# Kernel optimization log

Hardware: AMD Instinct MI355X
Metric: run time of the kernel (lower is better)

## Reference

```python
import jax, jax.numpy as jnp
import numpy as np

B, C, H, W = 4, 64, 64, 64  # x shape; mask is (B,1,8H,8W)


def _conv(x, w, pad=0):
    return jax.lax.conv_general_dilated(
        x, w, (1, 1), [(pad, pad), (pad, pad)],
        dimension_numbers=('NCHW', 'OIHW', 'NCHW'))


def _inorm(x, eps=1e-5):  # InstanceNorm2d, affine=False, biased var (torch default)
    mu = x.mean(axis=(2, 3), keepdims=True)
    var = x.var(axis=(2, 3), keepdims=True)
    return (x - mu) * jax.lax.rsqrt(var + eps)


def _forward(x, mask, kconv_w1, kconv_w2, fs_w1, fs_w2, fs_b2, fs_fuse_w):
    b, c, h, w = x.shape
    n = h * w
    # MaxPool2d(8,8) then binarize
    m = jax.lax.reduce_window(mask, -jnp.inf, jax.lax.max,
                              (1, 1, 8, 8), (1, 1, 8, 8), 'VALID')
    m = (m > 0).astype(x.dtype)
    back = 1.0 - m
    # ResidualBlock K_conv (shared for K and Q paths in original code)
    y = jax.nn.relu(_inorm(_conv(x, kconv_w1, pad=1)))
    y = _inorm(_conv(y, kconv_w2, pad=1))
    kx = jax.nn.relu(y + x)
    # L2-normalized K/Q over channel dim
    K = (kx * back).reshape(b, c, n)
    K = K / (jnp.linalg.norm(K, axis=1, keepdims=True) + 1e-8)
    Q = (kx * m).reshape(b, c, n)
    Q = Q / (jnp.linalg.norm(Q, axis=1, keepdims=True) + 1e-8)
    V = (x * back).reshape(b, c, n)
    # cosine-similarity score map, temperature 20
    score = jnp.einsum('bcq,bck->bqk', Q, K) * 20.0  # (b, n_q, n_k)
    qm = m.reshape(b, 1, n)      # query mask (foreground)
    km = back.reshape(b, 1, n)   # key mask (background)
    NEG = -1000000.0
    validx = score + (1.0 - km) * NEG + (1.0 - qm.transpose(0, 2, 1)) * NEG
    att = jax.nn.softmax(validx, axis=-1) * (qm.transpose(0, 2, 1) * km)
    # att_fore[b,c,q] = sum_k V[b,c,k] * att[b,q,k]
    att_fore = jnp.einsum('bck,bqk->bcq', V, att).reshape(b, c, h, w)
    # Fusion_score
    feat1 = _conv(jnp.concatenate([x * m, att_fore * m], axis=1), fs_w1)
    s = jax.nn.sigmoid(_conv(feat1, fs_w2) + fs_b2[None, :, None, None])
    fused = _conv(jnp.concatenate([x * m, att_fore * m * (1.0 - s)], axis=1), fs_fuse_w)
    fs_out = fused * m + x * (1.0 - m)
    out = fs_out * m + x * (1.0 - m)
    # visualization attention mask
    visatt = att.sum(axis=1).reshape(b, 1, h, w)
    attmask = jnp.repeat(jnp.repeat(visatt, 8, axis=2), 8, axis=3)  # nearest upsample x8
    attmask = attmask / attmask.max()
    return out, attmask


def setup_inputs() -> dict:
    key = jax.random.key(0)
    ks = jax.random.split(key, 8)

    def wgt(k, shape, fan_in):
        return jax.random.normal(k, shape, jnp.float32) / np.sqrt(fan_in)

    x = jax.random.normal(ks[0], (B, C, H, W), jnp.float32)
    # sparse foreground mask so maxpool(8x8)>0 yields a mixed fg/bg mask
    mask = (jax.random.uniform(ks[1], (B, 1, H * 8, W * 8)) < 0.01).astype(jnp.float32)
    return dict(
        x=x, mask=mask,
        kconv_w1=wgt(ks[2], (C, C, 3, 3), C * 9),
        kconv_w2=wgt(ks[3], (C, C, 3, 3), C * 9),
        fs_w1=wgt(ks[4], (C, 2 * C, 1, 1), 2 * C),
        fs_w2=wgt(ks[5], (C, C, 1, 1), C),
        fs_b2=jnp.zeros((C,), jnp.float32),
        fs_fuse_w=wgt(ks[6], (C, 2 * C, 1, 1), 2 * C),
    )


def reference(x, mask, kconv_w1, kconv_w2, fs_w1, fs_w2, fs_b2, fs_fuse_w):
    return _forward(x, mask, kconv_w1, kconv_w2, fs_w1, fs_w2, fs_b2, fs_fuse_w)
```

## Files before the change

### kernel.cpp

```cpp
#include <hip/hip_runtime.h>
#include <hip/hip_bf16.h>

typedef __hip_bfloat16 bf16;
typedef __attribute__((ext_vector_type(8))) short short8;
typedef __attribute__((ext_vector_type(4))) float f32x4;
typedef __attribute__((ext_vector_type(16))) float f32x16;

#define BB 4
#define CC 64
#define NN 4096
#define MH 512
#define MW 512
#define LS 72
#define NPARTS 16
#define NDEN 16

#define WB_AFC  ((size_t)0)
#define WB_VIS  ((size_t)4259840)
#define WB_QIX  ((size_t)4325376)
#define WB_KIX  ((size_t)4390912)
#define WB_MFL  ((size_t)4456448)
#define WB_CNT  ((size_t)4472832)
#define WB_WT1  ((size_t)4476992)
#define WB_WT2  ((size_t)4550720)
#define WB_WFB  ((size_t)4624448)
#define WB_KC   ((size_t)5242880)
#define WB_XT   ((size_t)8388608)
#define WB_KXT  ((size_t)10485760)
#define WB_VC   ((size_t)12582912)
#define WB_QC   ((size_t)14680064)
#define WB_E    ((size_t)16777216)
#define EB_ELEM ((size_t)16777216)
#define WB_AFCP ((size_t)150994944)
#define WB_DENP ((size_t)218103808)
#define WB_VISP ((size_t)220200960)
#define WB_GST  ((size_t)220725248)

__device__ __forceinline__ float us2f(unsigned short u) { return __uint_as_float(((unsigned)u) << 16); }
__device__ __forceinline__ unsigned short f2bu(float f) {
  bf16 h = __float2bfloat16(f);
  return *(unsigned short*)&h;
}

__global__ __launch_bounds__(256) void k_pre(const float* __restrict__ x,
                                             const float* __restrict__ mask,
                                             const float* __restrict__ w1,
                                             const float* __restrict__ w2,
                                             const float* __restrict__ fw1,
                                             const float* __restrict__ fw2,
                                             const float* __restrict__ fwf,
                                             float* __restrict__ outp,
                                             unsigned short* __restrict__ xt,
                                             unsigned char* __restrict__ mfl,
                                             float* __restrict__ vis,
                                             unsigned int* __restrict__ vmaxb,
                                             unsigned short* __restrict__ wT1,
                                             unsigned short* __restrict__ wT2,
                                             unsigned short* __restrict__ wfb) {
  __shared__ float lx[64][65];
  int t = threadIdx.x;
  if (blockIdx.x < 256) {
    int b = blockIdx.x >> 6, p0 = (blockIdx.x & 63) * 64;
    const float* xb = x + (size_t)b * CC * NN + p0;
    float* ob = outp + (size_t)b * CC * NN + p0;
    for (int idx = t; idx < 4096; idx += 256) {
      int c = idx >> 6, j = idx & 63;
      float v = xb[c * NN + j];
      lx[j][c] = v;
      ob[c * NN + j] = v;
    }
    __syncthreads();
    unsigned short* xo = xt + ((size_t)b * NN + p0) * 64;
    for (int idx = t; idx < 2048; idx += 256) {
      int j = idx >> 5, c2 = (idx & 31) * 2;
      ushort2 w2v;
      w2v.x = f2bu(lx[j][c2]);
      w2v.y = f2bu(lx[j][c2 + 1]);
      *(ushort2*)&xo[j * 64 + c2] = w2v;
    }
  } else {
    int g = (blockIdx.x - 256) * 256 + t;
    int o = g >> 2, sub = g & 3;
    int b = o >> 12, p = o & 4095;
    int py = p >> 6, px = p & 63;
    const float* mb = mask + (size_t)b * MH * MW + (py * 8 + sub * 2) * MW + px * 8;
    float mx = 0.f;
    #pragma unroll
    for (int dy = 0; dy < 2; ++dy) {
      const float4* r4 = (const float4*)(mb + dy * MW);
      float4 a = r4[0], c = r4[1];
      mx = fmaxf(mx, fmaxf(fmaxf(a.x, a.y), fmaxf(a.z, a.w)));
      mx = fmaxf(mx, fmaxf(fmaxf(c.x, c.y), fmaxf(c.z, c.w)));
    }
    mx = fmaxf(mx, __shfl_xor(mx, 1));
    mx = fmaxf(mx, __shfl_xor(mx, 2));
    if (sub == 0) {
      mfl[o] = (mx > 0.f) ? 1 : 0;
      vis[o] = 0.f;
    }
    if (g == 0) vmaxb[0] = 0u;
    if (g < 36864) {
      int tap = g >> 12;
      int rem = g & 4095;
      int co = rem >> 6, ci = rem & 63;
      int src = (co * 64 + ci) * 9 + tap;
      wT1[g] = f2bu(w1[src]);
      wT2[g] = f2bu(w2[src]);
    } else if (g < 57344) {
      int j2 = g - 36864;
      if (j2 < 8192)       wfb[j2] = f2bu(fw1[j2]);
      else if (j2 < 12288) wfb[j2] = f2bu(fw2[j2 - 8192]);
      else                 wfb[j2] = f2bu(fwf[j2 - 12288]);
    }
  }
}

__global__ __launch_bounds__(256) void k_compact(const unsigned char* __restrict__ mfl,
                                                 int* __restrict__ qidx, int* __restrict__ kidx,
                                                 int* __restrict__ nq, int* __restrict__ nk) {
  int b = blockIdx.x;
  __shared__ unsigned char lm[4096];
  int t = threadIdx.x;
  *(uint4*)&lm[t * 16] = *(const uint4*)&mfl[b * NN + t * 16];
  __syncthreads();
  if (t >= 64) return;
  int lane = t;
  int qb = 0, kb = 0;
  #pragma unroll
  for (int it = 0; it < 64; ++it) {
    int p = it * 64 + lane;
    bool f = lm[p] != 0;
    unsigned long long bal = __ballot(f);
    int before = __popcll(bal & ((1ULL << lane) - 1ULL));
    if (f)  qidx[b * NN + qb + before] = p;
    if (!f) kidx[b * NN + kb + (lane - before)] = p;
    int cnt = __popcll(bal);
    qb += cnt; kb += 64 - cnt;
  }
  if (lane == 0) { nq[b] = qb; nk[b] = kb; }
}

template <bool NORM_IN>
__global__ __launch_bounds__(256) void k_convm(const unsigned short* __restrict__ src,
                                               const unsigned short* __restrict__ wT,
                                               const float* __restrict__ insum,
                                               const float* __restrict__ insq,
                                               unsigned short* __restrict__ dst,
                                               float* __restrict__ gsump,
                                               float* __restrict__ gsqp) {
  int b = blockIdx.y;
  int r = blockIdx.x;
  __shared__ unsigned short bx[198 * LS];
  __shared__ float nmean[64], ninv[64];
  int t = threadIdx.x;
  if (NORM_IN) {
    if (t < 64) {
      float s = 0.f, s2v = 0.f;
      #pragma unroll 8
      for (int r2 = 0; r2 < 64; ++r2) {
        s   += insum[((size_t)r2 * BB + b) * 64 + t];
        s2v += insq [((size_t)r2 * BB + b) * 64 + t];
      }
      float m = s * (1.f / NN);
      float v = fmaxf(s2v * (1.f / NN) - m * m, 0.f);
      nmean[t] = m; ninv[t] = rsqrtf(v + 1e-5f);
    }
    __syncthreads();
  }
  const unsigned short* sb = src + (size_t)b * NN * 64;
  for (int idx = t; idx < 198 * 8; idx += 256) {
    int row = idx >> 3, c8 = (idx & 7) * 8;
    int dy = row / 66;
    int cx = row - dy * 66 - 1;
    int rr = r + dy - 1;
    uint4 v = make_uint4(0u, 0u, 0u, 0u);
    if ((unsigned)rr < 64u && (unsigned)cx < 64u) {
      v = *(const uint4*)(sb + ((size_t)(rr * 64 + cx)) * 64 + c8);
      if (NORM_IN) {
        unsigned short* e = (unsigned short*)&v;
        #pragma unroll
        for (int j = 0; j < 8; ++j)
          e[j] = f2bu(fmaxf((us2f(e[j]) - nmean[c8 + j]) * ninv[c8 + j], 0.f));
      }
    }
    *(uint4*)&bx[row * LS + c8] = v;
  }
  __syncthreads();
  int lane = t & 63;
  int quad = lane >> 4, col = lane & 15;
  int qw = (t >> 6) * 16;
  f32x4 acc[4] = {{0.f,0.f,0.f,0.f},{0.f,0.f,0.f,0.f},{0.f,0.f,0.f,0.f},{0.f,0.f,0.f,0.f}};
  #pragma unroll
  for (int tap = 0; tap < 9; ++tap) {
    int dy = tap / 3, dx = tap - dy * 3 - 1;
    const unsigned short* wrow = wT + ((size_t)tap * 64 + qw + col) * 64;
    short8 a0 = *(const short8*)(wrow + quad * 8);
    short8 a1 = *(const short8*)(wrow + 32 + quad * 8);
    int rbase = dy * 66 + dx + 1;
    #pragma unroll
    for (int nt = 0; nt < 4; ++nt) {
      int row = rbase + nt * 16 + col;
      short8 b0 = *(const short8*)&bx[row * LS + quad * 8];
      short8 b1 = *(const short8*)&bx[row * LS + 32 + quad * 8];
      acc[nt] = __builtin_amdgcn_mfma_f32_16x16x32_bf16(a0, b0, acc[nt], 0, 0, 0);
      acc[nt] = __builtin_amdgcn_mfma_f32_16x16x32_bf16(a1, b1, acc[nt], 0, 0, 0);
    }
  }
  #pragma unroll
  for (int rr = 0; rr < 4; ++rr) {
    float s1 = acc[0][rr] + acc[1][rr] + acc[2][rr] + acc[3][rr];
    float s2 = acc[0][rr]*acc[0][rr] + acc[1][rr]*acc[1][rr]
             + acc[2][rr]*acc[2][rr] + acc[3][rr]*acc[3][rr];
    s1 += __shfl_xor(s1, 1); s2 += __shfl_xor(s2, 1);
    s1 += __shfl_xor(s1, 2); s2 += __shfl_xor(s2, 2);
    s1 += __shfl_xor(s1, 4); s2 += __shfl_xor(s2, 4);
    s1 += __shfl_xor(s1, 8); s2 += __shfl_xor(s2, 8);
    if (col == 0) {
      int co = qw + quad * 4 + rr;
      gsump[((size_t)r * BB + b) * 64 + co] = s1;
      gsqp [((size_t)r * BB + b) * 64 + co] = s2;
    }
  }
  __syncthreads();
  #pragma unroll
  for (int nt = 0; nt < 4; ++nt)
    #pragma unroll
    for (int rr = 0; rr < 4; ++rr)
      bx[(nt * 16 + col) * LS + qw + quad * 4 + rr] = f2bu(acc[nt][rr]);
  __syncthreads();
  unsigned short* db = dst + ((size_t)b * NN + r * 64) * 64;
  for (int idx = t; idx < 512; idx += 256) {
    int px = idx >> 3, c8 = (idx & 7) * 8;
    *(uint4*)(db + (size_t)px * 64 + c8) = *(const uint4*)&bx[px * LS + c8];
  }
}

__global__ __launch_bounds__(256) void k_knorm(unsigned short* __restrict__ kxt,
                                               const unsigned short* __restrict__ xt,
                                               const float* __restrict__ gsump,
                                               const float* __restrict__ gsqp) {
  int b = blockIdx.x >> 6;
  int p0 = (blockIdx.x & 63) * 64;
  __shared__ float m2[64], i2[64];
  int t = threadIdx.x;
  if (t < 64) {
    float s = 0.f, s2v = 0.f;
    #pragma unroll 8
    for (int r2 = 0; r2 < 64; ++r2) {
      s   += gsump[((size_t)r2 * BB + b) * 64 + t];
      s2v += gsqp [((size_t)r2 * BB + b) * 64 + t];
    }
    float m = s * (1.f / NN);
    float v = fmaxf(s2v * (1.f / NN) - m * m, 0.f);
    m2[t] = m; i2[t] = rsqrtf(v + 1e-5f);
  }
  __syncthreads();
  int px = t >> 2, c0 = (t & 3) * 16;
  size_t base = ((size_t)b * NN + p0 + px) * 64 + c0;
  unsigned short kv[16], xv[16];
  *(uint4*)&kv[0] = *(const uint4*)(kxt + base);
  *(uint4*)&kv[8] = *(const uint4*)(kxt + base + 8);
  *(uint4*)&xv[0] = *(const uint4*)(xt + base);
  *(uint4*)&xv[8] = *(const uint4*)(xt + base + 8);
  float v[16]; float ss = 0.f;
  #pragma unroll
  for (int j = 0; j < 16; ++j) {
    float f = fmaxf((us2f(kv[j]) - m2[c0 + j]) * i2[c0 + j] + us2f(xv[j]), 0.f);
    v[j] = f; ss += f * f;
  }
  ss += __shfl_xor(ss, 1);
  ss += __shfl_xor(ss, 2);
  float inv = 1.f / (sqrtf(ss) + 1e-8f);
  #pragma unroll
  for (int j = 0; j < 16; ++j) kv[j] = f2bu(v[j] * inv);
  *(uint4*)(kxt + base) = *(const uint4*)&kv[0];
  *(uint4*)(kxt + base + 8) = *(const uint4*)&kv[8];
}

__global__ __launch_bounds__(256) void k_gath(const unsigned short* __restrict__ khat,
                                              const unsigned short* __restrict__ xt,
                                              const int* __restrict__ qidx, const int* __restrict__ kidx,
                                              const int* __restrict__ nqv, const int* __restrict__ nkv,
                                              unsigned short* __restrict__ kc,
                                              unsigned short* __restrict__ vc,
                                              unsigned short* __restrict__ qc) {
  int b = blockIdx.y;
  int j0 = blockIdx.x * 64;
  int nqb = nqv[b], nkb = nkv[b];
  int NKP = (nkb + 63) & ~63, NQP = (nqb + 63) & ~63;
  bool dok = j0 < NKP, doq = j0 < NQP;
  if (!dok && !doq) return;
  __shared__ int li[128];
  int t = threadIdx.x;
  if (t < 64) li[t] = (j0 + t < nkb) ? kidx[b * NN + j0 + t] : -1;
  if (t >= 64 && t < 128) li[t] = (j0 + (t - 64) < nqb) ? qidx[b * NN + j0 + (t - 64)] : -1;
  __syncthreads();
  const unsigned short* khb = khat + (size_t)b * NN * 64;
  const unsigned short* xtb = xt + (size_t)b * NN * 64;
  uint4 z = make_uint4(0u, 0u, 0u, 0u);
  for (int idx = t; idx < 512; idx += 256) {
    int row = idx >> 3, c8 = (idx & 7) * 8;
    size_t dsto = ((size_t)b * NN + j0 + row) * 64 + c8;
    if (dok) {
      int sk = li[row];
      *(uint4*)(kc + dsto) = (sk >= 0) ? *(const uint4*)(khb + (size_t)sk * 64 + c8) : z;
      *(uint4*)(vc + dsto) = (sk >= 0) ? *(const uint4*)(xtb + (size_t)sk * 64 + c8) : z;
    }
    if (doq) {
      int sq = li[64 + row];
      *(uint4*)(qc + dsto) = (sq >= 0) ? *(const uint4*)(khb + (size_t)sq * 64 + c8) : z;
    }
  }
}

__global__ __launch_bounds__(64) void k_att1(const unsigned short* __restrict__ kc,
                                             const unsigned short* __restrict__ vc,
                                             const unsigned short* __restrict__ qc,
                                             const int* __restrict__ nqv, const int* __restrict__ nkv,
                                             unsigned short* __restrict__ afc_part,
                                             float* __restrict__ den_part,
                                             unsigned short* __restrict__ eg) {
  int b = blockIdx.y;
  int nqb = nqv[b], nkb = nkv[b];
  int q0 = (blockIdx.x >> 4) * 32;
  int part = blockIdx.x & (NPARTS - 1);
  if (q0 >= nqb) return;
  int ntiles = (nkb + 63) >> 6;
  int nt_blk = (part < ntiles) ? ((ntiles - part + NPARTS - 1) >> 4) : 0;
  int NKP = (nkb + 63) & ~63;
  __shared__ unsigned short lk [64 * LS];
  __shared__ unsigned short lvT[64 * LS];
  __shared__ unsigned short le [32 * LS];
  int lane = threadIdx.x;
  int l31 = lane & 31, lhi = lane >> 5;
  const unsigned short* kcb = kc + (size_t)b * NN * 64;
  const unsigned short* vcb = vc + (size_t)b * NN * 64;
  const unsigned short* qcb = qc + (size_t)b * NN * 64;
  unsigned short* egb = eg + (size_t)b * EB_ELEM;
  unsigned short* afcp = afc_part + (((size_t)part * BB + b) * NN) * 64;
  float* denp = den_part + ((size_t)part * BB + b) * NN;
  short8 aq[4];
  #pragma unroll
  for (int ks = 0; ks < 4; ++ks)
    aq[ks] = *(const short8*)(qcb + (size_t)(q0 + l31) * 64 + ks * 16 + lhi * 8);
  f32x16 pv0, pv1, dsum;
  #pragma unroll
  for (int i = 0; i < 16; ++i) { pv0[i] = 0.f; pv1[i] = 0.f; dsum[i] = 0.f; }
  for (int it = 0; it < nt_blk; ++it) {
    int j0 = (part + it * NPARTS) * 64;
    #pragma unroll
    for (int sub = 0; sub < 4; ++sub) {
      int tt = sub * 64 + lane;
      int klo = tt >> 3, c8 = (tt & 7) * 8, vcc = tt & 7;
      *(uint4*)&lk[klo * LS + c8] = *(const uint4*)(kcb + (size_t)(j0 + klo) * 64 + c8);
      *(uint4*)&lk[(klo + 32) * LS + c8] = *(const uint4*)(kcb + (size_t)(j0 + klo + 32) * 64 + c8);
      uint4 v0 = *(const uint4*)(vcb + (size_t)(j0 + 2 * klo) * 64 + c8);
      uint4 v1 = *(const uint4*)(vcb + (size_t)(j0 + 2 * klo + 1) * 64 + c8);
      const unsigned short* e0 = (const unsigned short*)&v0;
      const unsigned short* e1 = (const unsigned short*)&v1;
      int pp = (klo & 3) + (((klo >> 2) ^ vcc) << 2);
      #pragma unroll
      for (int jj = 0; jj < 8; ++jj) {
        unsigned int w2 = (unsigned)e0[jj] | ((unsigned)e1[jj] << 16);
        *(unsigned int*)&lvT[(c8 + jj) * LS + pp * 2] = w2;
      }
    }
    #pragma unroll
    for (int kh = 0; kh < 2; ++kh) {
      f32x16 s;
      #pragma unroll
      for (int i = 0; i < 16; ++i) s[i] = 0.f;
      #pragma unroll
      for (int ks = 0; ks < 4; ++ks) {
        short8 bk = *(const short8*)&lk[(kh * 32 + l31) * LS + ks * 16 + lhi * 8];
        s = __builtin_amdgcn_mfma_f32_32x32x16_bf16(aq[ks], bk, s, 0, 0, 0);
      }
      bool kval = (j0 + kh * 32 + l31) < nkb;
      #pragma unroll
      for (int reg = 0; reg < 16; ++reg) {
        float e = kval ? __expf(20.f * s[reg]) : 0.f;
        dsum[reg] += e;
        int row = (reg & 3) + 8 * (reg >> 2) + 4 * lhi;
        le[row * LS + kh * 32 + l31] = f2bu(e);
      }
    }
    #pragma unroll
    for (int sub = 0; sub < 4; ++sub) {
      int idx = sub * 64 + lane;
      int q = idx >> 3, cc8 = (idx & 7) * 8;
      if (q0 + q < nqb)
        *(uint4*)(egb + (size_t)(q0 + q) * NKP + j0 + cc8) = *(const uint4*)&le[q * LS + cc8];
    }
    #pragma unroll
    for (int ch = 0; ch < 2; ++ch) {
      int c = ch * 32 + l31;
      int c37 = (c >> 3) & 7;
      #pragma unroll
      for (int ks = 0; ks < 4; ++ks) {
        short8 a  = *(const short8*)&le[l31 * LS + ks * 16 + lhi * 8];
        int run = ks * 2 + lhi;
        short8 bv = *(const short8*)&lvT[c * LS + ((run ^ c37) << 3)];
        if (ch == 0) pv0 = __builtin_amdgcn_mfma_f32_32x32x16_bf16(a, bv, pv0, 0, 0, 0);
        else         pv1 = __builtin_amdgcn_mfma_f32_32x32x16_bf16(a, bv, pv1, 0, 0, 0);
      }
    }
  }
  #pragma unroll
  for (int reg = 0; reg < 16; ++reg) {
    float v = dsum[reg];
    v += __shfl_xor(v, 1); v += __shfl_xor(v, 2); v += __shfl_xor(v, 4);
    v += __shfl_xor(v, 8); v += __shfl_xor(v, 16);
    int row = (reg & 3) + 8 * (reg >> 2) + 4 * lhi;
    int qq = q0 + row;
    if (l31 == 0 && qq < nqb) denp[qq] = v;
  }
  #pragma unroll
  for (int reg = 0; reg < 16; ++reg) {
    int row = (reg & 3) + 8 * (reg >> 2) + 4 * lhi;
    int qq = q0 + row;
    if (qq < nqb) {
      afcp[(size_t)qq * 64 + l31]      = f2bu(pv0[reg]);
      afcp[(size_t)qq * 64 + 32 + l31] = f2bu(pv1[reg]);
    }
  }
}

__global__ __launch_bounds__(256) void k_vis(const unsigned short* __restrict__ eg,
                                             const float* __restrict__ den_part,
                                             const int* __restrict__ nqv, const int* __restrict__ nkv,
                                             float* __restrict__ visp) {
  int b = blockIdx.z;
  int nqb = nqv[b], nkb = nkv[b];
  int k0 = blockIdx.x * 256;
  if (k0 >= nkb) return;
  int NKP = (nkb + 63) & ~63;
  int qpart = blockIdx.y;
  int qbeg = (qpart * nqb) >> 3;
  int qend = ((qpart + 1) * nqb) >> 3;
  __shared__ float wd[256];
  int t = threadIdx.x;
  int k = k0 + t;
  const unsigned short* eb = eg + (size_t)b * EB_ELEM;
  float acc = 0.f;
  for (int qc = qbeg; qc < qend; qc += 256) {
    __syncthreads();
    int qq = qc + t;
    float d = 0.f;
    if (qq < qend) {
      #pragma unroll
      for (int p2 = 0; p2 < NDEN; ++p2) d += den_part[((size_t)p2 * BB + b) * NN + qq];
    }
    wd[t] = (d > 0.f) ? 1.f / d : 0.f;
    __syncthreads();
    int lim = min(256, qend - qc);
    if (k < nkb) {
      const unsigned short* ep = eb + (size_t)qc * NKP + k;
      int j = 0;
      for (; j + 8 <= lim; j += 8) {
        #pragma unroll
        for (int u = 0; u < 8; ++u)
          acc += us2f(ep[(size_t)(j + u) * NKP]) * wd[j + u];
      }
      for (; j < lim; ++j)
        acc += us2f(ep[(size_t)j * NKP]) * wd[j];
    }
  }
  if (k < nkb) visp[((size_t)qpart * BB + b) * NN + k] = acc;
}

#define FS 136
__global__ __launch_bounds__(256) void k_fusionm(const unsigned short* __restrict__ xt,
                                                 const unsigned short* __restrict__ afc_part,
                                                 const float* __restrict__ den_part,
                                                 const int* __restrict__ qidx, const int* __restrict__ nqv,
                                                 const unsigned short* __restrict__ wall,
                                                 const float* __restrict__ b2,
                                                 float* __restrict__ outp) {
  int b = blockIdx.y;
  int nqb = nqv[b];
  int q0 = blockIdx.x * 64;
  if (q0 >= nqb) return;
  __shared__ unsigned short pxa[64 * FS];
  __shared__ unsigned short f1s[64 * LS];
  __shared__ int qpl[64];
  int t = threadIdx.x;
  int lane = t & 63;
  int quad = lane >> 4, col = lane & 15;
  int cb = (t >> 6) * 16;
  const int* qix = qidx + b * NN;
  const unsigned short* xtb = xt + (size_t)b * NN * 64;
  const unsigned short* w1b = wall;
  const unsigned short* w2b = wall + 8192;
  const unsigned short* wfb = wall + 12288;
  short8 a1[4], a2[2], af[4];
  #pragma unroll
  for (int kt = 0; kt < 4; ++kt) {
    a1[kt] = *(const short8*)&w1b[(cb + col) * 128 + kt * 32 + quad * 8];
    af[kt] = *(const short8*)&wfb[(cb + col) * 128 + kt * 32 + quad * 8];
  }
  #pragma unroll
  for (int kt = 0; kt < 2; ++kt)
    a2[kt] = *(const short8*)&w2b[(cb + col) * 64 + kt * 32 + quad * 8];
  float b2v[4];
  #pragma unroll
  for (int r = 0; r < 4; ++r) b2v[r] = b2[cb + quad * 4 + r];
  if (t < 64) qpl[t] = (q0 + t < nqb) ? qix[q0 + t] : -1;
  for (int idx = t; idx < 512; idx += 256) {
    int q = idx >> 3, c8 = (idx & 7) * 8;
    int qq = q0 + q;
    uint4 pv = make_uint4(0u, 0u, 0u, 0u);
    unsigned short pa8[8] = {0, 0, 0, 0, 0, 0, 0, 0};
    if (qq < nqb) {
      int qp = qix[qq];
      pv = *(const uint4*)(xtb + (size_t)qp * 64 + c8);
      float d = 0.f;
      #pragma unroll
      for (int p2 = 0; p2 < NDEN; ++p2)
        d += den_part[((size_t)p2 * BB + b) * NN + qq];
      float av[8];
      #pragma unroll
      for (int j = 0; j < 8; ++j) av[j] = 0.f;
      #pragma unroll
      for (int p2 = 0; p2 < NPARTS; ++p2) {
        const uint4 u = *(const uint4*)(afc_part + (((size_t)p2 * BB + b) * NN + qq) * 64 + c8);
        const unsigned short* e8 = (const unsigned short*)&u;
        #pragma unroll
        for (int j = 0; j < 8; ++j) av[j] += us2f(e8[j]);
      }
      float invd = (d > 0.f) ? 1.f / d : 0.f;
      #pragma unroll
      for (int j = 0; j < 8; ++j) pa8[j] = f2bu(av[j] * invd);
    }
    *(uint4*)&pxa[q * FS + c8] = pv;
    *(uint4*)&pxa[q * FS + 64 + c8] = *(const uint4*)&pa8[0];
  }
  __syncthreads();
  #pragma unroll
  for (int qt = 0; qt < 4; ++qt) {
    f32x4 acc = {0.f, 0.f, 0.f, 0.f};
    #pragma unroll
    for (int kt = 0; kt < 4; ++kt) {
      short8 bfrag = *(const short8*)&pxa[(qt * 16 + col) * FS + kt * 32 + quad * 8];
      acc = __builtin_amdgcn_mfma_f32_16x16x32_bf16(a1[kt], bfrag, acc, 0, 0, 0);
    }
    #pragma unroll
    for (int r = 0; r < 4; ++r)
      f1s[(qt * 16 + col) * LS + cb + quad * 4 + r] = f2bu(acc[r]);
  }
  __syncthreads();
  #pragma unroll
  for (int qt = 0; qt < 4; ++qt) {
    f32x4 acc = {0.f, 0.f, 0.f, 0.f};
    #pragma unroll
    for (int kt = 0; kt < 2; ++kt) {
      short8 bfrag = *(const short8*)&f1s[(qt * 16 + col) * LS + kt * 32 + quad * 8];
      acc = __builtin_amdgcn_mfma_f32_16x16x32_bf16(a2[kt], bfrag, acc, 0, 0, 0);
    }
    #pragma unroll
    for (int r = 0; r < 4; ++r) {
      float sg = 1.f / (1.f + __expf(-(acc[r] + b2v[r])));
      int addr = (qt * 16 + col) * FS + 64 + cb + quad * 4 + r;
      pxa[addr] = f2bu(us2f(pxa[addr]) * (1.f - sg));
    }
  }
  __syncthreads();
  #pragma unroll
  for (int qt = 0; qt < 4; ++qt) {
    f32x4 acc = {0.f, 0.f, 0.f, 0.f};
    #pragma unroll
    for (int kt = 0; kt < 4; ++kt) {
      short8 bfrag = *(const short8*)&pxa[(qt * 16 + col) * FS + kt * 32 + quad * 8];
      acc = __builtin_amdgcn_mfma_f32_16x16x32_bf16(af[kt], bfrag, acc, 0, 0, 0);
    }
    int qp = qpl[qt * 16 + col];
    if (qp >= 0) {
      #pragma unroll
      for (int r = 0; r < 4; ++r)
        outp[((size_t)b * CC + cb + quad * 4 + r) * NN + qp] = acc[r];
    }
  }
}

__global__ __launch_bounds__(256) void k_vmax(const float* __restrict__ visp,
                                              const int* __restrict__ kidx,
                                              const int* __restrict__ nkv,
                                              float* __restrict__ vis,
                                              unsigned int* __restrict__ vmaxb) {
  int i = blockIdx.x * 256 + threadIdx.x;
  int b = i >> 12, k = i & 4095;
  float v = 0.f;
  if (k < nkv[b]) {
    #pragma unroll
    for (int p2 = 0; p2 < 8; ++p2) v += visp[((size_t)p2 * BB + b) * NN + k];
    vis[b * NN + kidx[b * NN + k]] = v;
  }
  #pragma unroll
  for (int off = 32; off > 0; off >>= 1) v = fmaxf(v, __shfl_down(v, off));
  if ((threadIdx.x & 63) == 0) atomicMax(vmaxb, __float_as_uint(v));
}

__global__ __launch_bounds__(256) void k_upsample(const float* __restrict__ vis,
                                                  const unsigned int* __restrict__ vmaxb,
                                                  float* __restrict__ out2) {
  int i4 = blockIdx.x * 256 + threadIdx.x;
  int b = i4 >> 16;
  int rem = i4 & 65535;
  int y = rem >> 7, x4 = (rem & 127) * 4;
  float vm = __uint_as_float(vmaxb[0]);
  if (!(vm > 0.f)) vm = 1.f;
  float v = vis[b * NN + (y >> 3) * 64 + (x4 >> 3)] / vm;
  ((float4*)out2)[i4] = make_float4(v, v, v, v);
}

extern "C" void kernel_launch(void* const* d_in, const int* in_sizes, int n_in,
                              void* d_out, int out_size, void* d_ws, size_t ws_size,
                              hipStream_t stream) {
  const float* x    = (const float*)d_in[0];
  const float* mask = (const float*)d_in[1];
  const float* w1   = (const float*)d_in[2];
  const float* w2c  = (const float*)d_in[3];
  const float* fsw1 = (const float*)d_in[4];
  const float* fsw2 = (const float*)d_in[5];
  const float* fsb2 = (const float*)d_in[6];
  const float* fswf = (const float*)d_in[7];
  float* out = (float*)d_out;
  char* wsb = (char*)d_ws;

  float* vis = (float*)(wsb + WB_VIS);
  int* qidx  = (int*)(wsb + WB_QIX);
  int* kidx  = (int*)(wsb + WB_KIX);
  unsigned char* mfl = (unsigned char*)(wsb + WB_MFL);
  int* nq = (int*)(wsb + WB_CNT);
  int* nk = nq + 4;
  unsigned int* vmaxb = (unsigned int*)(nq + 8);
  unsigned short* wT1 = (unsigned short*)(wsb + WB_WT1);
  unsigned short* wT2 = (unsigned short*)(wsb + WB_WT2);
  unsigned short* wall = (unsigned short*)(wsb + WB_WFB);
  unsigned short* y1t = (unsigned short*)(wsb + WB_AFC);
  unsigned short* xt  = (unsigned short*)(wsb + WB_XT);
  unsigned short* kxt = (unsigned short*)(wsb + WB_KXT);
  unsigned short* khat = kxt;
  unsigned short* kc  = (unsigned short*)(wsb + WB_KC);
  unsigned short* vc  = (unsigned short*)(wsb + WB_VC);
  unsigned short* qc  = (unsigned short*)(wsb + WB_QC);
  unsigned short* eg  = (unsigned short*)(wsb + WB_E);
  unsigned short* afc_part = (unsigned short*)(wsb + WB_AFCP);
  float* den_part = (float*)(wsb + WB_DENP);
  float* visp     = (float*)(wsb + WB_VISP);
  float* gsum1p = (float*)(wsb + WB_GST);
  float* gsq1p  = (float*)(wsb + WB_GST + 65536);
  float* gsum2p = (float*)(wsb + WB_GST + 131072);
  float* gsq2p  = (float*)(wsb + WB_GST + 196608);

  k_pre<<<512, 256, 0, stream>>>(x, mask, w1, w2c, fsw1, fsw2, fswf,
                                 out, xt, mfl, vis, vmaxb, wT1, wT2, wall);
  k_compact<<<4, 256, 0, stream>>>(mfl, qidx, kidx, nq, nk);
  k_convm<false><<<dim3(64, BB), 256, 0, stream>>>(xt, wT1, nullptr, nullptr, y1t, gsum1p, gsq1p);
  k_convm<true><<<dim3(64, BB), 256, 0, stream>>>(y1t, wT2, gsum1p, gsq1p, kxt, gsum2p, gsq2p);
  k_knorm<<<256, 256, 0, stream>>>(kxt, xt, gsum2p, gsq2p);
  k_gath<<<dim3(64, BB), 256, 0, stream>>>(khat, xt, qidx, kidx, nq, nk, kc, vc, qc);
  k_att1<<<dim3(128 * NPARTS, BB), 64, 0, stream>>>(kc, vc, qc, nq, nk, afc_part, den_part, eg);
  k_vis<<<dim3(16, 8, BB), 256, 0, stream>>>(eg, den_part, nq, nk, visp);
  k_fusionm<<<dim3(64, BB), 256, 0, stream>>>(xt, afc_part, den_part, qidx, nq, wall, fsb2, out);
  k_vmax<<<64, 256, 0, stream>>>(visp, kidx, nk, vis, vmaxb);
  k_upsample<<<1024, 256, 0, stream>>>(vis, vmaxb, out + 1048576);
}
```

Before: 172.6 us.

## Pre-transpose V in gather kernel and read K/V operands directly from global

The gather kernel now writes V channel-major (c, key) through a shared-memory transpose, so the attention kernel can load MFMA B operands for the PV product straight from global memory. The attention kernel also reads K rows directly from global instead of staging them in LDS, which removes the per-tile LDS staging, swizzle and repacking. This cuts LDS traffic and shared-memory footprint, which could allow more waves per CU. The cost is strided global loads (4096-element stride for V rows) served by cache rather than LDS, plus an extra transpose step in the gather kernel.

After: 178.2 us. +3.3%, slower.

```diff
diff --git a/kernel.cpp b/kernel.cpp
--- a/kernel.cpp
+++ b/kernel.cpp
@@ -27,7 +27,7 @@
 #define WB_KC   ((size_t)5242880)
 #define WB_XT   ((size_t)8388608)
 #define WB_KXT  ((size_t)10485760)
-#define WB_VC   ((size_t)12582912)
+#define WB_VT   ((size_t)12582912)
 #define WB_QC   ((size_t)14680064)
 #define WB_E    ((size_t)16777216)
 #define EB_ELEM ((size_t)16777216)
@@ -282,7 +282,7 @@
                                               const int* __restrict__ qidx, const int* __restrict__ kidx,
                                               const int* __restrict__ nqv, const int* __restrict__ nkv,
                                               unsigned short* __restrict__ kc,
-                                              unsigned short* __restrict__ vc,
+                                              unsigned short* __restrict__ vt,
                                               unsigned short* __restrict__ qc) {
   int b = blockIdx.y;
   int j0 = blockIdx.x * 64;
@@ -291,6 +291,7 @@
   bool dok = j0 < NKP, doq = j0 < NQP;
   if (!dok && !doq) return;
   __shared__ int li[128];
+  __shared__ unsigned short tv[64 * LS];
   int t = threadIdx.x;
   if (t < 64) li[t] = (j0 + t < nkb) ? kidx[b * NN + j0 + t] : -1;
   if (t >= 64 && t < 128) li[t] = (j0 + (t - 64) < nqb) ? qidx[b * NN + j0 + (t - 64)] : -1;
@@ -304,17 +305,26 @@
     if (dok) {
       int sk = li[row];
       *(uint4*)(kc + dsto) = (sk >= 0) ? *(const uint4*)(khb + (size_t)sk * 64 + c8) : z;
-      *(uint4*)(vc + dsto) = (sk >= 0) ? *(const uint4*)(xtb + (size_t)sk * 64 + c8) : z;
+      *(uint4*)&tv[row * LS + c8] = (sk >= 0) ? *(const uint4*)(xtb + (size_t)sk * 64 + c8) : z;
     }
     if (doq) {
       int sq = li[64 + row];
       *(uint4*)(qc + dsto) = (sq >= 0) ? *(const uint4*)(khb + (size_t)sq * 64 + c8) : z;
     }
   }
+  __syncthreads();
+  if (!dok) return;
+  for (int idx = t; idx < 512; idx += 256) {
+    int c = idx >> 3, k8 = (idx & 7) * 8;
+    unsigned short vals[8];
+    #pragma unroll
+    for (int j = 0; j < 8; ++j) vals[j] = tv[(k8 + j) * LS + c];
+    *(uint4*)(vt + (size_t)b * 262144 + (size_t)c * 4096 + j0 + k8) = *(const uint4*)&vals[0];
+  }
 }
 
 __global__ __launch_bounds__(64) void k_att1(const unsigned short* __restrict__ kc,
-                                             const unsigned short* __restrict__ vc,
+                                             const unsigned short* __restrict__ vt,
                                              const unsigned short* __restrict__ qc,
                                              const int* __restrict__ nqv, const int* __restrict__ nkv,
                                              unsigned short* __restrict__ afc_part,
@@ -328,13 +338,11 @@
   int ntiles = (nkb + 63) >> 6;
   int nt_blk = (part < ntiles) ? ((ntiles - part + NPARTS - 1) >> 4) : 0;
   int NKP = (nkb + 63) & ~63;
-  __shared__ unsigned short lk [64 * LS];
-  __shared__ unsigned short lvT[64 * LS];
-  __shared__ unsigned short le [32 * LS];
+  __shared__ unsigned short le[32 * LS];
   int lane = threadIdx.x;
   int l31 = lane & 31, lhi = lane >> 5;
   const unsigned short* kcb = kc + (size_t)b * NN * 64;
-  const unsigned short* vcb = vc + (size_t)b * NN * 64;
+  const unsigned short* vtb = vt + (size_t)b * 262144;
   const unsigned short* qcb = qc + (size_t)b * NN * 64;
   unsigned short* egb = eg + (size_t)b * EB_ELEM;
   unsigned short* afcp = afc_part + (((size_t)part * BB + b) * NN) * 64;
@@ -349,30 +357,14 @@
   for (int it = 0; it < nt_blk; ++it) {
     int j0 = (part + it * NPARTS) * 64;
     #pragma unroll
-    for (int sub = 0; sub < 4; ++sub) {
-      int tt = sub * 64 + lane;
-      int klo = tt >> 3, c8 = (tt & 7) * 8, vcc = tt & 7;
-      *(uint4*)&lk[klo * LS + c8] = *(const uint4*)(kcb + (size_t)(j0 + klo) * 64 + c8);
-      *(uint4*)&lk[(klo + 32) * LS + c8] = *(const uint4*)(kcb + (size_t)(j0 + klo + 32) * 64 + c8);
-      uint4 v0 = *(const uint4*)(vcb + (size_t)(j0 + 2 * klo) * 64 + c8);
-      uint4 v1 = *(const uint4*)(vcb + (size_t)(j0 + 2 * klo + 1) * 64 + c8);
-      const unsigned short* e0 = (const unsigned short*)&v0;
-      const unsigned short* e1 = (const unsigned short*)&v1;
-      int pp = (klo & 3) + (((klo >> 2) ^ vcc) << 2);
-      #pragma unroll
-      for (int jj = 0; jj < 8; ++jj) {
-        unsigned int w2 = (unsigned)e0[jj] | ((unsigned)e1[jj] << 16);
-        *(unsigned int*)&lvT[(c8 + jj) * LS + pp * 2] = w2;
-      }
-    }
-    #pragma unroll
     for (int kh = 0; kh < 2; ++kh) {
       f32x16 s;
       #pragma unroll
       for (int i = 0; i < 16; ++i) s[i] = 0.f;
+      const unsigned short* krow = kcb + (size_t)(j0 + kh * 32 + l31) * 64 + lhi * 8;
       #pragma unroll
       for (int ks = 0; ks < 4; ++ks) {
-        short8 bk = *(const short8*)&lk[(kh * 32 + l31) * LS + ks * 16 + lhi * 8];
+        short8 bk = *(const short8*)(krow + ks * 16);
         s = __builtin_amdgcn_mfma_f32_32x32x16_bf16(aq[ks], bk, s, 0, 0, 0);
       }
       bool kval = (j0 + kh * 32 + l31) < nkb;
@@ -392,17 +384,12 @@
         *(uint4*)(egb + (size_t)(q0 + q) * NKP + j0 + cc8) = *(const uint4*)&le[q * LS + cc8];
     }
     #pragma unroll
-    for (int ch = 0; ch < 2; ++ch) {
-      int c = ch * 32 + l31;
-      int c37 = (c >> 3) & 7;
-      #pragma unroll
-      for (int ks = 0; ks < 4; ++ks) {
-        short8 a  = *(const short8*)&le[l31 * LS + ks * 16 + lhi * 8];
-        int run = ks * 2 + lhi;
-        short8 bv = *(const short8*)&lvT[c * LS + ((run ^ c37) << 3)];
-        if (ch == 0) pv0 = __builtin_amdgcn_mfma_f32_32x32x16_bf16(a, bv, pv0, 0, 0, 0);
-        else         pv1 = __builtin_amdgcn_mfma_f32_32x32x16_bf16(a, bv, pv1, 0, 0, 0);
-      }
+    for (int ks = 0; ks < 4; ++ks) {
+      short8 a = *(const short8*)&le[l31 * LS + ks * 16 + lhi * 8];
+      short8 bv0 = *(const short8*)(vtb + (size_t)l31 * 4096 + j0 + ks * 16 + lhi * 8);
+      short8 bv1 = *(const short8*)(vtb + (size_t)(32 + l31) * 4096 + j0 + ks * 16 + lhi * 8);
+      pv0 = __builtin_amdgcn_mfma_f32_32x32x16_bf16(a, bv0, pv0, 0, 0, 0);
+      pv1 = __builtin_amdgcn_mfma_f32_32x32x16_bf16(a, bv1, pv1, 0, 0, 0);
     }
   }
   #pragma unroll
@@ -641,7 +628,7 @@
   unsigned short* kxt = (unsigned short*)(wsb + WB_KXT);
   unsigned short* khat = kxt;
   unsigned short* kc  = (unsigned short*)(wsb + WB_KC);
-  unsigned short* vc  = (unsigned short*)(wsb + WB_VC);
+  unsigned short* vt  = (unsigned short*)(wsb + WB_VT);
   unsigned short* qc  = (unsigned short*)(wsb + WB_QC);
   unsigned short* eg  = (unsigned short*)(wsb + WB_E);
   unsigned short* afc_part = (unsigned short*)(wsb + WB_AFCP);
@@ -658,8 +645,8 @@
   k_convm<false><<<dim3(64, BB), 256, 0, stream>>>(xt, wT1, nullptr, nullptr, y1t, gsum1p, gsq1p);
   k_convm<true><<<dim3(64, BB), 256, 0, stream>>>(y1t, wT2, gsum1p, gsq1p, kxt, gsum2p, gsq2p);
   k_knorm<<<256, 256, 0, stream>>>(kxt, xt, gsum2p, gsq2p);
-  k_gath<<<dim3(64, BB), 256, 0, stream>>>(khat, xt, qidx, kidx, nq, nk, kc, vc, qc);
-  k_att1<<<dim3(128 * NPARTS, BB), 64, 0, stream>>>(kc, vc, qc, nq, nk, afc_part, den_part, eg);
+  k_gath<<<dim3(64, BB), 256, 0, stream>>>(khat, xt, qidx, kidx, nq, nk, kc, vt, qc);
+  k_att1<<<dim3(128 * NPARTS, BB), 64, 0, stream>>>(kc, vt, qc, nq, nk, afc_part, den_part, eg);
   k_vis<<<dim3(16, 8, BB), 256, 0, stream>>>(eg, den_part, nq, nk, visp);
   k_fusionm<<<dim3(64, BB), 256, 0, stream>>>(xt, afc_part, den_part, qidx, nq, wall, fsb2, out);
   k_vmax<<<64, 256, 0, stream>>>(visp, kidx, nk, vis, vmaxb);
```
